# Performance work log

Measured on AMD Instinct MI355X. Metric: run time of the kernel, lower is better.

Reference implementation:

```python
import jax, jax.numpy as jnp
import numpy as np

DIM = 4096
N_HEADS = 32
N_KV_HEADS = 8
HEAD_DIM = 128
EPS = 1e-6
SEQ = 2048
N_SEG = 4
SEG_LEN = SEQ // N_SEG


def setup_inputs() -> dict:
    key = jax.random.key(0)
    ks = jax.random.split(key, 6)
    s = 0.02
    x = jax.random.normal(ks[0], (1, SEQ, DIM), jnp.float32)
    wq = jax.random.normal(ks[1], (N_HEADS * HEAD_DIM, DIM), jnp.float32) * s
    wk = jax.random.normal(ks[2], (N_KV_HEADS * HEAD_DIM, DIM), jnp.float32) * s
    wv = jax.random.normal(ks[3], (N_KV_HEADS * HEAD_DIM, DIM), jnp.float32) * s
    wo = jax.random.normal(ks[4], (DIM, N_HEADS * HEAD_DIM), jnp.float32) * s
    q_norm_w = jnp.ones((HEAD_DIM,), jnp.float32)
    k_norm_w = jnp.ones((HEAD_DIM,), jnp.float32)
    # RoPE cache: [max_pos, head_dim//2, 2] = (cos, sin)
    inv_freq = 1.0 / (10000.0 ** (jnp.arange(0, HEAD_DIM // 2, dtype=jnp.float32) / (HEAD_DIM // 2)))
    t = jnp.arange(SEQ, dtype=jnp.float32)
    freqs = jnp.outer(t, inv_freq)  # [SEQ, hd/2]
    rope_cache = jnp.stack([jnp.cos(freqs), jnp.sin(freqs)], axis=-1)
    # packed varlen: 4 segments of 512, positions restart per segment
    positions = (jnp.arange(SEQ, dtype=jnp.int32) % SEG_LEN)[None, :]
    cu_seqlens = jnp.arange(N_SEG + 1, dtype=jnp.int32) * SEG_LEN
    return {"x": x, "wq": wq, "wk": wk, "wv": wv, "wo": wo,
            "q_norm_w": q_norm_w, "k_norm_w": k_norm_w,
            "rope_cache": rope_cache, "positions": positions,
            "cu_seqlens": cu_seqlens}


def _rms_norm(x, w):
    xf = x.astype(jnp.float32)
    var = jnp.mean(xf * xf, axis=-1, keepdims=True)
    return w * (xf * jax.lax.rsqrt(var + EPS))


def _apply_rope(x, rope_cache, positions):
    # x: [bs, S, h, hd]; rope_cache: [P, hd/2, 2]; positions: [bs, S]
    cs = rope_cache[positions]                    # [bs, S, hd/2, 2]
    cos = cs[..., 0][:, :, None, :]               # [bs, S, 1, hd/2]
    sin = cs[..., 1][:, :, None, :]
    half = x.shape[-1] // 2
    x1, x2 = x[..., :half], x[..., half:]
    return jnp.concatenate([x1 * cos - x2 * sin, x2 * cos + x1 * sin], axis=-1)


def reference(x, wq, wk, wv, wo, q_norm_w, k_norm_w, rope_cache, positions, cu_seqlens):
    bs, S, _ = x.shape
    n_rep = N_HEADS // N_KV_HEADS
    xq = (x @ wq.T).reshape(bs, S, N_HEADS, HEAD_DIM)
    xk = (x @ wk.T).reshape(bs, S, N_KV_HEADS, HEAD_DIM)
    xv = (x @ wv.T).reshape(bs, S, N_KV_HEADS, HEAD_DIM)
    xq = _rms_norm(xq, q_norm_w)
    xk = _rms_norm(xk, k_norm_w)
    xq = _apply_rope(xq, rope_cache, positions)
    xk = _apply_rope(xk, rope_cache, positions)
    # GQA: repeat kv heads
    xk = jnp.repeat(xk, n_rep, axis=2)
    xv = jnp.repeat(xv, n_rep, axis=2)
    q = xq.transpose(0, 2, 1, 3)  # [bs, h, S, hd]
    k = xk.transpose(0, 2, 1, 3)
    v = xv.transpose(0, 2, 1, 3)
    # varlen mask: causal within each packed segment
    idx = jnp.arange(S)
    seg = jnp.searchsorted(cu_seqlens, idx, side='right') - 1  # [S]
    mask = (seg[:, None] == seg[None, :]) & (idx[:, None] >= idx[None, :])
    scale = HEAD_DIM ** -0.5
    scores = jnp.einsum('bhqd,bhkd->bhqk', q, k) * scale
    scores = jnp.where(mask[None, None], scores, jnp.float32(-1e30))
    probs = jax.nn.softmax(scores, axis=-1)
    out = jnp.einsum('bhqk,bhkd->bhqd', probs, v)
    out = out.transpose(0, 2, 1, 3).reshape(bs, S, N_HEADS * HEAD_DIM)
    return out @ wo.T
```

## Files before the change

kernel.cpp:

```cpp
#include <hip/hip_runtime.h>

typedef __bf16 bf16_t;
typedef __bf16 bf16x8 __attribute__((ext_vector_type(8)));
typedef __bf16 bf16x4 __attribute__((ext_vector_type(4)));
typedef float f32x4 __attribute__((ext_vector_type(4)));

#define SEQL 2048
#define DIMM 4096
#define NH 32
#define NKV 8
#define HD 128

__device__ __forceinline__ void gl2lds16(const void* g, void* l) {
  __builtin_amdgcn_global_load_lds((__attribute__((address_space(1))) void*)g,
                                   (__attribute__((address_space(3))) void*)l,
                                   16, 0, 0);
}

__global__ __launch_bounds__(256) void cvt5_kernel(const float* __restrict__ s0,
                                                   const float* __restrict__ s1,
                                                   const float* __restrict__ s2,
                                                   const float* __restrict__ s3,
                                                   const float* __restrict__ s4,
                                                   bf16_t* __restrict__ dst) {
  const long base = (long)blockIdx.x * 4096;
  const float* s;
  long o;
  if (base < 8388608L)       { s = s0; o = base; }
  else if (base < 25165824L) { s = s1; o = base - 8388608L; }
  else if (base < 29360128L) { s = s2; o = base - 25165824L; }
  else if (base < 33554432L) { s = s3; o = base - 29360128L; }
  else                       { s = s4; o = base - 33554432L; }
  const long t4 = threadIdx.x * 4;
#pragma unroll
  for (int j = 0; j < 4; ++j) {
    const long e = t4 + j * 1024;
    float4 v = *(const float4*)(s + o + e);
    bf16x4 ov;
    ov[0] = (bf16_t)v.x; ov[1] = (bf16_t)v.y; ov[2] = (bf16_t)v.z; ov[3] = (bf16_t)v.w;
    *(bf16x4*)(dst + base + e) = ov;
  }
}

#define TS 136
#define QSCALE (0.08838834764831845f * 1.4426950408889634f)
__global__ __launch_bounds__(256, 3) void gemm_qkv_kernel(const bf16_t* __restrict__ A,
                                                          const bf16_t* __restrict__ B,
                                                          const float* __restrict__ qnw,
                                                          const float* __restrict__ knw,
                                                          const float* __restrict__ rope,
                                                          const int* __restrict__ pos,
                                                          bf16_t* __restrict__ Qb,
                                                          bf16_t* __restrict__ Kb,
                                                          bf16_t* __restrict__ Vb) {
  __shared__ __align__(16) bf16_t smem[128 * TS];
  bf16_t* lA = smem;
  bf16_t* lB = smem + 8192;
  const int K = DIMM, npanel = 6;
  const int tid = threadIdx.x;
  const int lin = blockIdx.x;
  const int xcd = lin & 7, idx = lin >> 3;
  const int bm = (idx & 15) * 128;
  const int bn = ((idx >> 4) + xcd * npanel) * 128;
  const int lane = tid & 63, wave = tid >> 6;
  const int wm = (wave >> 1) * 64, wn = (wave & 1) * 64;
  const int lr = lane & 15, quad = lane >> 4;

  f32x4 acc[4][4];
#pragma unroll
  for (int mi = 0; mi < 4; ++mi)
#pragma unroll
    for (int ni = 0; ni < 4; ++ni)
      acc[mi][ni] = (f32x4){0.f, 0.f, 0.f, 0.f};

  long soff[4];
#pragma unroll
  for (int c = 0; c < 4; ++c) {
    const int s = tid + 256 * c;
    soff[c] = (long)(s >> 3) * K + (((s & 7) ^ ((s >> 3) & 7)) << 3);
  }
  const bf16_t* Abase = A + (long)bm * K;
  const bf16_t* Bbase = B + (long)bn * K;

  for (int k0 = 0; k0 < K; k0 += 64) {
    __syncthreads();
#pragma unroll
    for (int c = 0; c < 4; ++c) {
      gl2lds16(Abase + soff[c] + k0, lA + (tid + 256 * c) * 8);
      gl2lds16(Bbase + soff[c] + k0, lB + (tid + 256 * c) * 8);
    }
    __syncthreads();
#pragma unroll
    for (int ks = 0; ks < 2; ++ks) {
      bf16x8 af[4], bfr[4];
#pragma unroll
      for (int mi = 0; mi < 4; ++mi)
        af[mi] = *(const bf16x8*)&lA[(wm + mi * 16 + lr) * 64 + ((((ks << 2) | quad) ^ (lr & 7)) << 3)];
#pragma unroll
      for (int ni = 0; ni < 4; ++ni)
        bfr[ni] = *(const bf16x8*)&lB[(wn + ni * 16 + lr) * 64 + ((((ks << 2) | quad) ^ (lr & 7)) << 3)];
#pragma unroll
      for (int mi = 0; mi < 4; ++mi)
#pragma unroll
        for (int ni = 0; ni < 4; ++ni)
          acc[mi][ni] = __builtin_amdgcn_mfma_f32_16x16x32_bf16(af[mi], bfr[ni], acc[mi][ni], 0, 0, 0);
    }
  }

  __syncthreads();
  bf16_t* tile = smem;
#pragma unroll
  for (int mi = 0; mi < 4; ++mi)
#pragma unroll
    for (int ni = 0; ni < 4; ++ni)
#pragma unroll
      for (int r = 0; r < 4; ++r)
        tile[(wm + mi * 16 + quad * 4 + r) * TS + wn + ni * 16 + lr] = (bf16_t)acc[mi][ni][r];
  __syncthreads();

  if (bn < 5120) {
    const bool isQ = bn < 4096;
    const float* nwp = isQ ? qnw : knw;
    const float osc = isQ ? QSCALE : 1.0f;
    bf16_t* outp = isQ ? (Qb + (long)(bn >> 7) * SEQL * HD)
                       : (Kb + (long)((bn - 4096) >> 7) * SEQL * HD);
    const int r = tid >> 1, hf = tid & 1;
    bf16x8 rowv[16];
#pragma unroll
    for (int j = 0; j < 16; ++j) rowv[j] = *(const bf16x8*)&tile[r * TS + j * 8];
    float ss = 0.f;
#pragma unroll
    for (int j = 0; j < 16; ++j)
#pragma unroll
      for (int e = 0; e < 8; ++e) { const float f = (float)rowv[j][e]; ss += f * f; }
    const float sc = rsqrtf(ss * (1.0f / 128.0f) + 1e-6f) * osc;
    const int p = pos[bm + r];
    const float* rp = rope + p * 128;
    bf16_t obuf[64];
#pragma unroll
    for (int g = 0; g < 8; ++g) {
#pragma unroll
      for (int e = 0; e < 8; ++e) {
        const int i = g * 8 + e;
        const float2 cs = *(const float2*)(rp + 2 * i);
        const float nlo = (float)rowv[i >> 3][i & 7] * sc * nwp[i];
        const float nhi = (float)rowv[8 + (i >> 3)][i & 7] * sc * nwp[64 + i];
        obuf[i] = (bf16_t)(hf ? (nhi * cs.x + nlo * cs.y) : (nlo * cs.x - nhi * cs.y));
      }
    }
    bf16_t* op = outp + (long)(bm + r) * HD + hf * 64;
#pragma unroll
    for (int g = 0; g < 8; ++g) *(bf16x8*)(op + g * 8) = *(const bf16x8*)&obuf[g * 8];
  } else {
    const int hk = (bn - 5120) >> 7;
    const int d = tid & 127, shalf = tid >> 7;
    bf16_t* vp = Vb + ((long)hk * HD + d) * SEQL + bm + shalf * 64;
#pragma unroll
    for (int grp = 0; grp < 8; ++grp) {
      bf16x8 t;
#pragma unroll
      for (int e = 0; e < 8; ++e) t[e] = tile[(shalf * 64 + grp * 8 + e) * TS + d];
      *(bf16x8*)(vp + grp * 8) = t;
    }
  }
}

template <typename CT>
__global__ __launch_bounds__(256, 3) void gemm_bt_kernel(const bf16_t* __restrict__ A,
                                                         const bf16_t* __restrict__ B,
                                                         CT* __restrict__ C,
                                                         int N, int K, int npanel) {
  __shared__ bf16_t lA[128 * 64];
  __shared__ bf16_t lB[128 * 64];
  const int tid = threadIdx.x;
  const int lin = blockIdx.x;
  const int xcd = lin & 7, idx = lin >> 3;
  const int bm = (idx & 15) * 128;
  const int bn = ((idx >> 4) + xcd * npanel) * 128;
  const int lane = tid & 63, wave = tid >> 6;
  const int wm = (wave >> 1) * 64, wn = (wave & 1) * 64;
  const int lr = lane & 15, quad = lane >> 4;

  f32x4 acc[4][4];
#pragma unroll
  for (int mi = 0; mi < 4; ++mi)
#pragma unroll
    for (int ni = 0; ni < 4; ++ni)
      acc[mi][ni] = (f32x4){0.f, 0.f, 0.f, 0.f};

  long soff[4];
#pragma unroll
  for (int c = 0; c < 4; ++c) {
    const int s = tid + 256 * c;
    soff[c] = (long)(s >> 3) * K + (((s & 7) ^ ((s >> 3) & 7)) << 3);
  }
  const bf16_t* Abase = A + (long)bm * K;
  const bf16_t* Bbase = B + (long)bn * K;

  for (int k0 = 0; k0 < K; k0 += 64) {
    __syncthreads();
#pragma unroll
    for (int c = 0; c < 4; ++c) {
      gl2lds16(Abase + soff[c] + k0, lA + (tid + 256 * c) * 8);
      gl2lds16(Bbase + soff[c] + k0, lB + (tid + 256 * c) * 8);
    }
    __syncthreads();
#pragma unroll
    for (int ks = 0; ks < 2; ++ks) {
      bf16x8 af[4], bfr[4];
#pragma unroll
      for (int mi = 0; mi < 4; ++mi)
        af[mi] = *(const bf16x8*)&lA[(wm + mi * 16 + lr) * 64 + ((((ks << 2) | quad) ^ (lr & 7)) << 3)];
#pragma unroll
      for (int ni = 0; ni < 4; ++ni)
        bfr[ni] = *(const bf16x8*)&lB[(wn + ni * 16 + lr) * 64 + ((((ks << 2) | quad) ^ (lr & 7)) << 3)];
#pragma unroll
      for (int mi = 0; mi < 4; ++mi)
#pragma unroll
        for (int ni = 0; ni < 4; ++ni)
          acc[mi][ni] = __builtin_amdgcn_mfma_f32_16x16x32_bf16(af[mi], bfr[ni], acc[mi][ni], 0, 0, 0);
    }
  }

#pragma unroll
  for (int mi = 0; mi < 4; ++mi) {
    const int row = bm + wm + mi * 16 + quad * 4;
#pragma unroll
    for (int ni = 0; ni < 4; ++ni) {
      const int col = bn + wn + ni * 16 + lr;
      CT* cp = C + (long)row * N + col;
#pragma unroll
      for (int r = 0; r < 4; ++r) cp[(long)r * N] = (CT)acc[mi][ni][r];
    }
  }
}

#define CK 64
#define PSTR 72
__global__ __launch_bounds__(256) void attn_kernel(const bf16_t* __restrict__ Q,
                                                   const bf16_t* __restrict__ Kt,
                                                   const bf16_t* __restrict__ Vt,
                                                   bf16_t* __restrict__ O) {
  __shared__ bf16_t lK[2 * CK * 128];
  __shared__ bf16_t lV[144 * CK];
  __shared__ bf16_t lP[128 * PSTR];
  const int lin = blockIdx.x;
  const int qb = (lin < 256) ? (3 - (lin & 1)) : (lin & 1);
  const int gh = (lin >> 1) & 127;
  const int h = gh & 31, g = gh >> 5;
  const int hk = h >> 2;
  const int tid = threadIdx.x, lane = tid & 63, wave = tid >> 6;
  const int lr = lane & 15, quad = lane >> 4;
  const int s_base = g * 512 + qb * 128;

  if (tid < 128) {
    bf16x8 one8;
#pragma unroll
    for (int j = 0; j < 8; ++j) one8[j] = (bf16_t)1.0f;
    *(bf16x8*)&lV[128 * CK + tid * 8] = one8;
  }

  bf16x8 qf[2][4];
  const bf16_t* Qp = Q + ((long)h * SEQL + s_base + wave * 32 + lr) * HD + quad * 8;
#pragma unroll
  for (int mi = 0; mi < 2; ++mi)
#pragma unroll
    for (int ks = 0; ks < 4; ++ks)
      qf[mi][ks] = *(const bf16x8*)(Qp + mi * 16 * HD + ks * 32);

  f32x4 oacc[2][9];
#pragma unroll
  for (int mi = 0; mi < 2; ++mi)
#pragma unroll
    for (int di = 0; di < 9; ++di) oacc[mi][di] = (f32x4){0.f, 0.f, 0.f, 0.f};

  const bf16_t* Kg0 = Kt + ((long)hk * SEQL + g * 512) * HD;
  const bf16_t* Vg0 = Vt + (long)hk * HD * SEQL + g * 512;

#define STGK(c_, buf_)                                                        \
  do {                                                                        \
    const bf16_t* Kg = Kg0 + (long)(c_) * CK * HD;                            \
    _Pragma("unroll")                                                         \
    for (int cc = 0; cc < 4; ++cc) {                                          \
      const int i = tid + 256 * cc;                                           \
      gl2lds16(Kg + (long)(i >> 4) * HD + (i & 15) * 8,                       \
               lK + (buf_) * (CK * 128) + i * 8);                             \
    }                                                                         \
  } while (0)
#define STGV(c_)                                                              \
  do {                                                                        \
    const bf16_t* Vg = Vg0 + (long)(c_) * CK;                                 \
    _Pragma("unroll")                                                         \
    for (int cc = 0; cc < 4; ++cc) {                                          \
      const int i = tid + 256 * cc;                                           \
      gl2lds16(Vg + (long)(i >> 3) * SEQL + (i & 7) * 8, lV + i * 8);         \
    }                                                                         \
  } while (0)

  const int nchunk = 2 * qb + 2;
  STGK(0, 0);
  STGV(0);

  for (int c = 0; c < nchunk; ++c) {
    __syncthreads();
    if (c > 0) STGV(c);
    if (c + 1 < nchunk) STGK(c + 1, (c + 1) & 1);
    if (c + 1 < nchunk) { asm volatile("s_waitcnt vmcnt(8)" ::: "memory"); }
    else                { asm volatile("s_waitcnt vmcnt(4)" ::: "memory"); }
    __syncthreads();

    const bf16_t* lKc = lK + (c & 1) * (CK * 128);
    f32x4 sv[2][4];
#pragma unroll
    for (int mi = 0; mi < 2; ++mi)
#pragma unroll
      for (int ni = 0; ni < 4; ++ni) sv[mi][ni] = (f32x4){0.f, 0.f, 0.f, 0.f};
    __builtin_amdgcn_s_setprio(1);
#pragma unroll
    for (int ks = 0; ks < 4; ++ks) {
#pragma unroll
      for (int ni = 0; ni < 4; ++ni) {
        const bf16x8 kf = *(const bf16x8*)&lKc[(ni * 16 + lr) * 128 + ks * 32 + quad * 8];
        sv[0][ni] = __builtin_amdgcn_mfma_f32_16x16x32_bf16(qf[0][ks], kf, sv[0][ni], 0, 0, 0);
        sv[1][ni] = __builtin_amdgcn_mfma_f32_16x16x32_bf16(qf[1][ks], kf, sv[1][ni], 0, 0, 0);
      }
    }
    __builtin_amdgcn_s_setprio(0);

#pragma unroll
    for (int mi = 0; mi < 2; ++mi)
#pragma unroll
      for (int ni = 0; ni < 4; ++ni)
#pragma unroll
        for (int r = 0; r < 4; ++r) {
          const int colseg = c * CK + ni * 16 + lr;
          const int rowseg = qb * 128 + wave * 32 + mi * 16 + quad * 4 + r;
          float p = exp2f(sv[mi][ni][r]);
          p = (colseg > rowseg) ? 0.f : p;
          lP[(wave * 32 + mi * 16 + quad * 4 + r) * PSTR + ni * 16 + lr] = (bf16_t)p;
        }
    if (c + 1 < nchunk) { asm volatile("s_waitcnt vmcnt(4)" ::: "memory"); }
    else                { asm volatile("s_waitcnt vmcnt(0)" ::: "memory"); }
    __syncthreads();

    __builtin_amdgcn_s_setprio(1);
#pragma unroll
    for (int ks = 0; ks < 2; ++ks) {
      const bf16x8 pf0 = *(const bf16x8*)&lP[(wave * 32 + lr) * PSTR + ks * 32 + quad * 8];
      const bf16x8 pf1 = *(const bf16x8*)&lP[(wave * 32 + 16 + lr) * PSTR + ks * 32 + quad * 8];
#pragma unroll
      for (int di = 0; di < 9; ++di) {
        const bf16x8 vfr = *(const bf16x8*)&lV[(di * 16 + lr) * CK + ks * 32 + quad * 8];
        oacc[0][di] = __builtin_amdgcn_mfma_f32_16x16x32_bf16(pf0, vfr, oacc[0][di], 0, 0, 0);
        oacc[1][di] = __builtin_amdgcn_mfma_f32_16x16x32_bf16(pf1, vfr, oacc[1][di], 0, 0, 0);
      }
    }
    __builtin_amdgcn_s_setprio(0);
  }
#undef STGK
#undef STGV

#pragma unroll
  for (int mi = 0; mi < 2; ++mi)
#pragma unroll
    for (int r = 0; r < 4; ++r) {
      const float inv = 1.0f / oacc[mi][8][r];
      const int row = s_base + wave * 32 + mi * 16 + quad * 4 + r;
      bf16_t* opp = O + (long)row * DIMM + h * HD + lr;
#pragma unroll
      for (int di = 0; di < 8; ++di) opp[di * 16] = (bf16_t)(oacc[mi][di][r] * inv);
    }
}

extern "C" void kernel_launch(void* const* d_in, const int* in_sizes, int n_in,
                              void* d_out, int out_size, void* d_ws, size_t ws_size,
                              hipStream_t stream) {
  (void)in_sizes; (void)n_in; (void)out_size; (void)ws_size;
  const float* x    = (const float*)d_in[0];
  const float* wq   = (const float*)d_in[1];
  const float* wk   = (const float*)d_in[2];
  const float* wv   = (const float*)d_in[3];
  const float* wo   = (const float*)d_in[4];
  const float* qnw  = (const float*)d_in[5];
  const float* knw  = (const float*)d_in[6];
  const float* rope = (const float*)d_in[7];
  const int*   pos  = (const int*)d_in[8];
  float* out = (float*)d_out;

  char* ws = (char*)d_ws;
  size_t off = 0;
  auto alloc = [&](size_t b) { char* p = ws + off; off += (b + 255) & ~(size_t)255; return p; };
  bf16_t* xb    = (bf16_t*)alloc((size_t)SEQL * DIMM * 2);
  bf16_t* wqkvb = (bf16_t*)alloc((size_t)DIMM * DIMM * 2);
  alloc((size_t)NKV * HD * DIMM * 2);
  alloc((size_t)NKV * HD * DIMM * 2);
  bf16_t* wob   = (bf16_t*)alloc((size_t)DIMM * DIMM * 2);
  bf16_t* Qb    = (bf16_t*)alloc((size_t)NH * SEQL * HD * 2);
  bf16_t* Kb    = (bf16_t*)alloc((size_t)NKV * SEQL * HD * 2);
  bf16_t* Vb    = (bf16_t*)alloc((size_t)NKV * SEQL * HD * 2);
  bf16_t* attnb = xb;

  cvt5_kernel<<<dim3(12288), 256, 0, stream>>>(x, wq, wk, wv, wo, xb);
  gemm_qkv_kernel<<<dim3(768), 256, 0, stream>>>(xb, wqkvb, qnw, knw, rope, pos, Qb, Kb, Vb);
  attn_kernel<<<dim3(512), 256, 0, stream>>>(Qb, Kb, Vb, attnb);
  gemm_bt_kernel<float><<<dim3(512), 256, 0, stream>>>(attnb, wob, out, DIMM, DIMM, 4);
}
```

Measured before the change: 425.4 us.

## Overlap wo fp32-to-bf16 conversion with QKV GEMM via interleaved extra blocks

Removes the wo weight conversion from the standalone convert kernel and runs it inside the QKV GEMM launch. Extra blocks are interleaved with the GEMM blocks (2 of every 5 per XCD group), and each converts a 32K-element chunk. The memory-bound conversion can then overlap the compute-bound GEMM instead of running serially before it. The risks are contention for bandwidth and CU slots with the GEMM tiles, and the remapped tile index changes which tiles share an XCD.

```diff
diff --git a/kernel.cpp b/kernel.cpp
--- a/kernel.cpp
+++ b/kernel.cpp
@@ -17,11 +17,10 @@
                                    16, 0, 0);
 }
 
-__global__ __launch_bounds__(256) void cvt5_kernel(const float* __restrict__ s0,
+__global__ __launch_bounds__(256) void cvt4_kernel(const float* __restrict__ s0,
                                                    const float* __restrict__ s1,
                                                    const float* __restrict__ s2,
                                                    const float* __restrict__ s3,
-                                                   const float* __restrict__ s4,
                                                    bf16_t* __restrict__ dst) {
   const long base = (long)blockIdx.x * 4096;
   const float* s;
@@ -29,8 +28,7 @@
   if (base < 8388608L)       { s = s0; o = base; }
   else if (base < 25165824L) { s = s1; o = base - 8388608L; }
   else if (base < 29360128L) { s = s2; o = base - 25165824L; }
-  else if (base < 33554432L) { s = s3; o = base - 29360128L; }
-  else                       { s = s4; o = base - 33554432L; }
+  else                       { s = s3; o = base - 29360128L; }
   const long t4 = threadIdx.x * 4;
 #pragma unroll
   for (int j = 0; j < 4; ++j) {
@@ -50,18 +48,35 @@
                                                           const float* __restrict__ knw,
                                                           const float* __restrict__ rope,
                                                           const int* __restrict__ pos,
+                                                          const float* __restrict__ wo_src,
+                                                          bf16_t* __restrict__ wo_dst,
                                                           bf16_t* __restrict__ Qb,
                                                           bf16_t* __restrict__ Kb,
                                                           bf16_t* __restrict__ Vb) {
+  const int p = blockIdx.x;
+  const int g = p >> 3, l8 = p & 7;
+  const int gq = g / 5, gr = g % 5;
+  if (gr >= 3) {
+    const long cb = ((long)(gq * 2 + (gr - 3)) * 8 + l8) * 32768;
+    const long t4 = threadIdx.x * 4;
+#pragma unroll 4
+    for (int j = 0; j < 32; ++j) {
+      const long e = cb + t4 + (long)j * 1024;
+      float4 v = *(const float4*)(wo_src + e);
+      bf16x4 ov;
+      ov[0] = (bf16_t)v.x; ov[1] = (bf16_t)v.y; ov[2] = (bf16_t)v.z; ov[3] = (bf16_t)v.w;
+      *(bf16x4*)(wo_dst + e) = ov;
+    }
+    return;
+  }
   __shared__ __align__(16) bf16_t smem[128 * TS];
   bf16_t* lA = smem;
   bf16_t* lB = smem + 8192;
-  const int K = DIMM, npanel = 6;
+  const int K = DIMM;
   const int tid = threadIdx.x;
-  const int lin = blockIdx.x;
-  const int xcd = lin & 7, idx = lin >> 3;
+  const int xcd = l8, idx = gq * 3 + gr;
   const int bm = (idx & 15) * 128;
-  const int bn = ((idx >> 4) + xcd * npanel) * 128;
+  const int bn = ((idx >> 4) + xcd * 6) * 128;
   const int lane = tid & 63, wave = tid >> 6;
   const int wm = (wave >> 1) * 64, wn = (wave & 1) * 64;
   const int lr = lane & 15, quad = lane >> 4;
@@ -134,14 +149,14 @@
 #pragma unroll
       for (int e = 0; e < 8; ++e) { const float f = (float)rowv[j][e]; ss += f * f; }
     const float sc = rsqrtf(ss * (1.0f / 128.0f) + 1e-6f) * osc;
-    const int p = pos[bm + r];
-    const float* rp = rope + p * 128;
+    const int pp = pos[bm + r];
+    const float* rp = rope + pp * 128;
     bf16_t obuf[64];
 #pragma unroll
-    for (int g = 0; g < 8; ++g) {
+    for (int gg = 0; gg < 8; ++gg) {
 #pragma unroll
       for (int e = 0; e < 8; ++e) {
-        const int i = g * 8 + e;
+        const int i = gg * 8 + e;
         const float2 cs = *(const float2*)(rp + 2 * i);
         const float nlo = (float)rowv[i >> 3][i & 7] * sc * nwp[i];
         const float nhi = (float)rowv[8 + (i >> 3)][i & 7] * sc * nwp[64 + i];
@@ -150,7 +165,7 @@
     }
     bf16_t* op = outp + (long)(bm + r) * HD + hf * 64;
 #pragma unroll
-    for (int g = 0; g < 8; ++g) *(bf16x8*)(op + g * 8) = *(const bf16x8*)&obuf[g * 8];
+    for (int gg = 0; gg < 8; ++gg) *(bf16x8*)(op + gg * 8) = *(const bf16x8*)&obuf[gg * 8];
   } else {
     const int hk = (bn - 5120) >> 7;
     const int d = tid & 127, shalf = tid >> 7;
@@ -400,8 +415,9 @@
   bf16_t* Vb    = (bf16_t*)alloc((size_t)NKV * SEQL * HD * 2);
   bf16_t* attnb = xb;
 
-  cvt5_kernel<<<dim3(12288), 256, 0, stream>>>(x, wq, wk, wv, wo, xb);
-  gemm_qkv_kernel<<<dim3(768), 256, 0, stream>>>(xb, wqkvb, qnw, knw, rope, pos, Qb, Kb, Vb);
+  cvt4_kernel<<<dim3(8192), 256, 0, stream>>>(x, wq, wk, wv, xb);
+  gemm_qkv_kernel<<<dim3(1280), 256, 0, stream>>>(xb, wqkvb, qnw, knw, rope, pos,
+                                                  wo, wob, Qb, Kb, Vb);
   attn_kernel<<<dim3(512), 256, 0, stream>>>(Qb, Kb, Vb, attnb);
   gemm_bt_kernel<float><<<dim3(512), 256, 0, stream>>>(attnb, wob, out, DIMM, DIMM, 4);
 }
```

New measurement: 463.4 us. 1.09x slower.
